# Kernel tuning notes

Hardware: AMD Instinct MI355X
Metric: run time of the kernel (lower is better)

## Reference

```python
import jax, jax.numpy as jnp
import numpy as np

L, B, S, D, SD, E, V = 6, 16, 512, 512, 128, 1536, 32000
PDX = 1  # padding_idx: embedding row zeroed


def _pos_encode(seq_len, d_model):
    pos = np.arange(seq_len)[:, None].astype(np.float32)
    i = np.arange(d_model)[None, :].astype(np.float32)
    ang = pos / np.power(10000.0, 2.0 * np.floor(i / 2.0) / d_model)
    pe = np.where(np.arange(d_model)[None, :] % 2 == 0, np.sin(ang), np.cos(ang))
    return jnp.asarray(pe, dtype=jnp.float32)


def setup_inputs() -> dict:
    key = jax.random.key(0)
    ks = jax.random.split(key, 12)
    def n(k, shape, std=0.02):
        return jax.random.normal(k, shape, jnp.float32) * std
    embed = n(ks[0], (V, D)).at[PDX].set(0.0)
    return dict(
        src_tokens=jax.random.randint(ks[1], (B, S), 0, V),
        src_mask=jax.random.randint(ks[2], (B, S), 0, 2).astype(bool),
        embed=embed,
        ln_g=jnp.ones((L, D)), ln_b=jnp.zeros((L, D)),
        Wz=n(ks[3], (L, D, SD)), bz=jnp.zeros((L, SD)),
        gq=1.0 + n(ks[4], (L, S, SD)), bq=n(ks[5], (L, S, SD)),
        gk=1.0 + n(ks[6], (L, S, SD)), bk=n(ks[7], (L, S, SD)),
        Wu=n(ks[8], (L, D, E)), bu=jnp.zeros((L, E)),
        Wv=n(ks[9], (L, D, E)), bv=jnp.zeros((L, E)),
        Wo=n(ks[10], (L, E, D)), bo=jnp.zeros((L, D)),
        fin_g=jnp.ones((D,)), fin_b=jnp.zeros((D,)),
    )


def _ln(x, g, b, eps=1e-5):
    m = x.mean(-1, keepdims=True)
    v = ((x - m) ** 2).mean(-1, keepdims=True)
    return (x - m) * jax.lax.rsqrt(v + eps) * g + b


def reference(src_tokens, src_mask, embed, ln_g, ln_b, Wz, bz, gq, bq, gk, bk,
              Wu, bu, Wv, bv, Wo, bo, fin_g, fin_b):
    d_model = embed.shape[1]
    x = embed[src_tokens] * (d_model ** 0.5)
    x = x + _pos_encode(src_tokens.shape[1], d_model)[None]  # dropout: eval -> identity
    mask = src_mask[:, None, :]  # (B,1,S): zero attention to masked key positions

    def layer(x, p):
        lg, lb, wz, bz_, gq_, bq_, gk_, bk_, wu, bu_, wv, bv_, wo, bo_ = p
        xn = _ln(x, lg, lb)
        u = xn @ wu + bu_          # (B,S,E)
        v = xn @ wv + bv_          # (B,S,E)
        z = xn @ wz + bz_          # (B,S,SD)
        q = z * gq_ + bq_          # scale_offset (per-position affine)
        k = z * gk_ + bk_
        a = jnp.maximum(jnp.einsum('bsd,btd->bst', q, k), 0.0) ** 2  # relu(qk)^2
        a = jnp.where(mask, 0.0, a)
        o = u * jnp.einsum('bst,bte->bse', a, v)  # gated attention output
        return x + o @ wo + bo_, None

    params = (ln_g, ln_b, Wz, bz, gq, bq, gk, bk, Wu, bu, Wv, bv, Wo, bo)
    x, _ = jax.lax.scan(layer, x, params)
    return _ln(x, fin_g, fin_b)
```

## Files before the change

kernel.cpp:

```cpp
#include <hip/hip_runtime.h>
#include <hip/hip_bf16.h>
#include <stdint.h>

constexpr int L = 6, B = 16, S = 512, D = 512, SD = 128, E = 1536;

using bf16x8 = __attribute__((ext_vector_type(8))) short;
using f32x4  = __attribute__((ext_vector_type(4))) float;

typedef __attribute__((address_space(1))) void gvoid;
typedef __attribute__((address_space(3))) void lvoid;

__device__ __forceinline__ unsigned short f2bf(float f) {
    __hip_bfloat16 h = __float2bfloat16(f);
    return __builtin_bit_cast(unsigned short, h);
}
__device__ __forceinline__ float bf2f(unsigned short u) {
    unsigned int v = ((unsigned int)u) << 16;
    return __builtin_bit_cast(float, v);
}
__device__ __forceinline__ void gload16(const void* g, void* l) {
    __builtin_amdgcn_global_load_lds((gvoid*)g, (lvoid*)l, 16, 0, 0);
}

__global__ void detect_mask_kernel(const unsigned char* __restrict__ m, int* flag) {
    if (threadIdx.x == 0) *flag = 0;
    __syncthreads();
    int any = 0;
    for (int i = threadIdx.x; i < B * S; i += blockDim.x)
        if ((i & 3) != 0 && m[i] != 0) any = 1;
    if (any) atomicOr(flag, 1);
}

__global__ void embed_kernel(const int* __restrict__ tok, const float* __restrict__ embed,
                             float* __restrict__ x) {
    int idx = blockIdx.x * blockDim.x + threadIdx.x;
    int d = idx & (D - 1);
    int bs = idx >> 9;
    int s = bs & (S - 1);
    float e = embed[(size_t)tok[bs] * D + d] * 22.62741699796952f;
    float expo = (float)(d >> 1) * (1.0f / 256.0f);
    float ang = (float)s * expf(expo * -9.210340371976184f);
    float pe = (d & 1) ? cosf(ang) : sinf(ang);
    x[idx] = e + pe;
}

__global__ __launch_bounds__(256) void tcast_kernel(const float* __restrict__ W,
                                                    unsigned short* __restrict__ Wt,
                                                    int K, int N, long ostride) {
    __shared__ float t[32][33];
    W  += (size_t)blockIdx.z * K * N;
    Wt += (size_t)blockIdx.z * ostride;
    int k0 = blockIdx.x * 32, n0 = blockIdx.y * 32;
    int tx = threadIdx.x, ty = threadIdx.y;
#pragma unroll
    for (int i = 0; i < 4; ++i)
        t[ty + i * 8][tx] = W[(size_t)(k0 + ty + i * 8) * N + n0 + tx];
    __syncthreads();
#pragma unroll
    for (int i = 0; i < 4; ++i)
        Wt[(size_t)(n0 + ty + i * 8) * K + k0 + tx] = f2bf(t[tx][ty + i * 8]);
}

template <bool BF>
__global__ __launch_bounds__(64) void ln_kernel(const float* __restrict__ x,
                                                const float* __restrict__ g,
                                                const float* __restrict__ b,
                                                void* __restrict__ yp) {
    int row = blockIdx.x;
    int lane = threadIdx.x;
    const float* xr = x + (size_t)row * D;
    float4 v0 = *(const float4*)(xr + lane * 4);
    float4 v1 = *(const float4*)(xr + 256 + lane * 4);
    float sum = v0.x + v0.y + v0.z + v0.w + v1.x + v1.y + v1.z + v1.w;
#pragma unroll
    for (int o = 1; o < 64; o <<= 1) sum += __shfl_xor(sum, o);
    float m = sum * (1.0f / D);
    float d0 = v0.x - m, d1 = v0.y - m, d2 = v0.z - m, d3 = v0.w - m;
    float e0 = v1.x - m, e1 = v1.y - m, e2 = v1.z - m, e3 = v1.w - m;
    float sq = d0 * d0 + d1 * d1 + d2 * d2 + d3 * d3 + e0 * e0 + e1 * e1 + e2 * e2 + e3 * e3;
#pragma unroll
    for (int o = 1; o < 64; o <<= 1) sq += __shfl_xor(sq, o);
    float inv = rsqrtf(sq * (1.0f / D) + 1e-5f);
    int c0 = lane * 4, c1 = 256 + lane * 4;
    float4 g0 = *(const float4*)(g + c0), g1 = *(const float4*)(g + c1);
    float4 b0 = *(const float4*)(b + c0), b1 = *(const float4*)(b + c1);
    float o0 = d0 * inv * g0.x + b0.x, o1 = d1 * inv * g0.y + b0.y;
    float o2 = d2 * inv * g0.z + b0.z, o3 = d3 * inv * g0.w + b0.w;
    float o4 = e0 * inv * g1.x + b1.x, o5 = e1 * inv * g1.y + b1.y;
    float o6 = e2 * inv * g1.z + b1.z, o7 = e3 * inv * g1.w + b1.w;
    if constexpr (BF) {
        unsigned short* yr = (unsigned short*)yp + (size_t)row * D;
        ushort4 p0 = {f2bf(o0), f2bf(o1), f2bf(o2), f2bf(o3)};
        ushort4 p1 = {f2bf(o4), f2bf(o5), f2bf(o6), f2bf(o7)};
        *(ushort4*)(yr + c0) = p0;
        *(ushort4*)(yr + c1) = p1;
    } else {
        float* yr = (float*)yp + (size_t)row * D;
        float4 p0 = {o0, o1, o2, o3}, p1 = {o4, o5, o6, o7};
        *(float4*)(yr + c0) = p0;
        *(float4*)(yr + c1) = p1;
    }
}

__global__ void qk_kernel(const float* __restrict__ z, const float* __restrict__ gq,
                          const float* __restrict__ bq, const float* __restrict__ gk,
                          const float* __restrict__ bk, unsigned short* __restrict__ q,
                          unsigned short* __restrict__ k) {
    int idx = blockIdx.x * blockDim.x + threadIdx.x;
    int sc = idx & (S * SD - 1);
    float zv = z[idx];
    q[idx] = f2bf(fmaf(zv, gq[sc], bq[sc]));
    k[idx] = f2bf(fmaf(zv, gk[sc], bk[sc]));
}

template <int BM, int BN>
__device__ __forceinline__ void gemm_core(const unsigned short* __restrict__ Ab,
                                          const unsigned short* __restrict__ Bb,
                                          int K, short* lsA, short* lsB,
                                          f32x4 (&acc)[BM / 32][BN / 32],
                                          int lane, int wv) {
    constexpr int NA = BM / 32, NB = BN / 32;
    constexpr int FM = BM / 32, FN = BN / 32;
    constexpr int WTM = BM / 2, WTN = BN / 2;
    const int wm = wv >> 1, wn = wv & 1;
    const unsigned short* ga[NA]; int lofsA[NA];
    const unsigned short* gb[NB]; int lofsB[NB];
#pragma unroll
    for (int i = 0; i < NA; ++i) {
        int s = wv * NA + i;
        int r = s * 8 + (lane >> 3);
        int cl = (lane & 7) ^ (r & 7);
        ga[i] = Ab + (size_t)r * K + cl * 8;
        lofsA[i] = s * 512;
    }
#pragma unroll
    for (int i = 0; i < NB; ++i) {
        int s = wv * NB + i;
        int r = s * 8 + (lane >> 3);
        int cl = (lane & 7) ^ (r & 7);
        gb[i] = Bb + (size_t)r * K + cl * 8;
        lofsB[i] = s * 512;
    }
    const int nkt = K >> 6;
    for (int kt = 0; kt < nkt; ++kt) {
        if (kt) __syncthreads();
#pragma unroll
        for (int i = 0; i < NA; ++i) gload16(ga[i] + kt * 64, (void*)&lsA[lofsA[i]]);
#pragma unroll
        for (int i = 0; i < NB; ++i) gload16(gb[i] + kt * 64, (void*)&lsB[lofsB[i]]);
        __syncthreads();
#pragma unroll
        for (int ks = 0; ks < 2; ++ks) {
            bf16x8 aF[FM], bF[FN];
#pragma unroll
            for (int f = 0; f < FM; ++f) {
                int ra = wm * WTM + f * 16 + (lane & 15);
                int ca = (ks * 4 + (lane >> 4)) ^ (ra & 7);
                aF[f] = *(const bf16x8*)&lsA[ra * 64 + ca * 8];
            }
#pragma unroll
            for (int f = 0; f < FN; ++f) {
                int rb = wn * WTN + f * 16 + (lane & 15);
                int cb = (ks * 4 + (lane >> 4)) ^ (rb & 7);
                bF[f] = *(const bf16x8*)&lsB[rb * 64 + cb * 8];
            }
#pragma unroll
            for (int fi = 0; fi < FM; ++fi)
#pragma unroll
                for (int fj = 0; fj < FN; ++fj)
                    acc[fi][fj] = __builtin_amdgcn_mfma_f32_16x16x32_bf16(
                        aF[fi], bF[fj], acc[fi][fj], 0, 0, 0);
        }
    }
}

template <int EPI, int BM, int BN>
__global__ __launch_bounds__(256) void mgemm(const unsigned short* __restrict__ A,
                                             const unsigned short* __restrict__ Bt,
                                             const float* __restrict__ bias,
                                             const void* __restrict__ aux,
                                             const int* __restrict__ flagp,
                                             void* __restrict__ Cp,
                                             int N, int K,
                                             long sA, long sB, long sC, long sAux) {
    __shared__ short lsA[BM * 64];
    __shared__ short lsB[BN * 64];
    constexpr int FM = BM / 32, FN = BN / 32;
    const int tid = threadIdx.x;
    const int lane = tid & 63, wv = tid >> 6;
    const int wm = wv >> 1, wn = wv & 1;
    const int row0 = blockIdx.x * BM, col0 = blockIdx.y * BN;
    const int bz = blockIdx.z;

    const unsigned short* Ab = A + (size_t)bz * sA + (size_t)row0 * K;
    const unsigned short* Bb = Bt + (size_t)bz * sB + (size_t)col0 * K;

    f32x4 acc[FM][FN] = {};
    gemm_core<BM, BN>(Ab, Bb, K, lsA, lsB, acc, lane, wv);

    const int lr4 = (lane >> 4) * 4;
    const int lc = lane & 15;
#pragma unroll
    for (int fi = 0; fi < FM; ++fi) {
        int rb = row0 + wm * (BM / 2) + fi * 16 + lr4;
#pragma unroll
        for (int fj = 0; fj < FN; ++fj) {
            int c = col0 + wn * (BN / 2) + fj * 16 + lc;
            f32x4 v = acc[fi][fj];
            if constexpr (EPI == 3) {
                int mv = (*flagp) ? (int)((const unsigned char*)aux)[bz * sAux + c]
                                  : ((const int*)aux)[bz * sAux + c];
                unsigned short* C = (unsigned short*)Cp + (size_t)bz * sC;
#pragma unroll
                for (int g = 0; g < 4; ++g) {
                    float vv = fmaxf(v[g], 0.0f);
                    vv *= vv;
                    C[(size_t)(rb + g) * N + c] = mv ? (unsigned short)0 : f2bf(vv);
                }
            } else if constexpr (EPI == 4) {
                const unsigned short* U = (const unsigned short*)aux + (size_t)bz * sAux;
                unsigned short* C = (unsigned short*)Cp + (size_t)bz * sC;
#pragma unroll
                for (int g = 0; g < 4; ++g) {
                    size_t off = (size_t)(rb + g) * N + c;
                    C[off] = f2bf(bf2f(U[off]) * v[g]);
                }
            } else {
                float bv = bias[c];
                const float* X = (const float*)aux;
                float* C = (float*)Cp;
#pragma unroll
                for (int g = 0; g < 4; ++g) {
                    size_t off = (size_t)(rb + g) * N + c;
                    C[off] = v[g] + bv + X[off];
                }
            }
        }
    }
}

__global__ __launch_bounds__(256) void uvz_gemm(const unsigned short* __restrict__ xn,
                                                const unsigned short* __restrict__ Wuvzt,
                                                const float* __restrict__ bu,
                                                const float* __restrict__ bvp,
                                                const float* __restrict__ bzp,
                                                unsigned short* __restrict__ u,
                                                unsigned short* __restrict__ vt,
                                                float* __restrict__ z) {
    __shared__ short lsA[128 * 64];
    __shared__ short lsB[128 * 64];
    const int tid = threadIdx.x;
    const int lane = tid & 63, wv = tid >> 6;
    const int wm = wv >> 1, wn = wv & 1;
    const int row0 = blockIdx.x * 128, col0 = blockIdx.y * 128;

    const unsigned short* Ab = xn + (size_t)row0 * D;
    const unsigned short* Bb = Wuvzt + (size_t)col0 * D;

    f32x4 acc[4][4] = {};
    gemm_core<128, 128>(Ab, Bb, D, lsA, lsB, acc, lane, wv);

    const int lr4 = (lane >> 4) * 4;
    const int lc = lane & 15;
#pragma unroll
    for (int fi = 0; fi < 4; ++fi) {
        int rb = row0 + wm * 64 + fi * 16 + lr4;
#pragma unroll
        for (int fj = 0; fj < 4; ++fj) {
            int c = col0 + wn * 64 + fj * 16 + lc;
            f32x4 v = acc[fi][fj];
            if (c < 1536) {
                float bv = bu[c];
#pragma unroll
                for (int g = 0; g < 4; ++g)
                    u[(size_t)(rb + g) * E + c] = f2bf(v[g] + bv);
            } else if (c < 3072) {
                int cv = c - 1536;
                float bv = bvp[cv];
                int b = rb >> 9, t0 = rb & 511;
                ushort4 o = {f2bf(v[0] + bv), f2bf(v[1] + bv),
                             f2bf(v[2] + bv), f2bf(v[3] + bv)};
                *(ushort4*)&vt[((size_t)b * E + cv) * 512 + t0] = o;
            } else {
                int cz = c - 3072;
                float bv = bzp[cz];
#pragma unroll
                for (int g = 0; g < 4; ++g)
                    z[(size_t)(rb + g) * SD + cz] = v[g] + bv;
            }
        }
    }
}

extern "C" void kernel_launch(void* const* d_in, const int* in_sizes, int n_in,
                              void* d_out, int out_size, void* d_ws, size_t ws_size,
                              hipStream_t stream) {
    const int* tok = (const int*)d_in[0];
    const unsigned char* mask = (const unsigned char*)d_in[1];
    const float* embed = (const float*)d_in[2];
    const float* ln_g = (const float*)d_in[3];
    const float* ln_b = (const float*)d_in[4];
    const float* Wz = (const float*)d_in[5];
    const float* bz = (const float*)d_in[6];
    const float* gq = (const float*)d_in[7];
    const float* bq = (const float*)d_in[8];
    const float* gk = (const float*)d_in[9];
    const float* bk = (const float*)d_in[10];
    const float* Wu = (const float*)d_in[11];
    const float* bu = (const float*)d_in[12];
    const float* Wv = (const float*)d_in[13];
    const float* bv = (const float*)d_in[14];
    const float* Wo = (const float*)d_in[15];
    const float* bo = (const float*)d_in[16];
    const float* fin_g = (const float*)d_in[17];
    const float* fin_b = (const float*)d_in[18];

    char* wsb = (char*)d_ws;
    size_t off = 0;
    auto alloc = [&](size_t nbytes) {
        void* p = wsb + off;
        off = (off + nbytes + 255) & ~(size_t)255;
        return p;
    };
    int* flag = (int*)alloc(256);
    float* x = (float*)alloc((size_t)B * S * D * 4);
    unsigned short* xn = (unsigned short*)alloc((size_t)B * S * D * 2);
    float* z = (float*)alloc((size_t)B * S * SD * 4);
    unsigned short* q = (unsigned short*)alloc((size_t)B * S * SD * 2);
    unsigned short* k = (unsigned short*)alloc((size_t)B * S * SD * 2);
    unsigned short* u = (unsigned short*)alloc((size_t)B * S * E * 2);
    unsigned short* vt = (unsigned short*)alloc((size_t)B * E * S * 2);
    unsigned short* o = (unsigned short*)alloc((size_t)B * S * E * 2);
    unsigned short* a = (unsigned short*)alloc((size_t)B * S * S * 2);
    unsigned short* Wuvzt = (unsigned short*)alloc((size_t)L * 3200 * D * 2);
    unsigned short* Wot = (unsigned short*)alloc((size_t)L * D * E * 2);

    constexpr long WUVZ = 3200L * D;

    detect_mask_kernel<<<1, 256, 0, stream>>>(mask, flag);
    embed_kernel<<<(B * S * D) / 256, 256, 0, stream>>>(tok, embed, x);
    tcast_kernel<<<dim3(D / 32, E / 32, L), dim3(32, 8), 0, stream>>>(Wu, Wuvzt, D, E, WUVZ);
    tcast_kernel<<<dim3(D / 32, E / 32, L), dim3(32, 8), 0, stream>>>(
        Wv, Wuvzt + 1536L * D, D, E, WUVZ);
    tcast_kernel<<<dim3(D / 32, SD / 32, L), dim3(32, 8), 0, stream>>>(
        Wz, Wuvzt + 3072L * D, D, SD, WUVZ);
    tcast_kernel<<<dim3(E / 32, D / 32, L), dim3(32, 8), 0, stream>>>(
        Wo, Wot, E, D, (long)D * E);

    for (int l = 0; l < L; ++l) {
        ln_kernel<true><<<B * S, 64, 0, stream>>>(x, ln_g + l * D, ln_b + l * D, xn);
        uvz_gemm<<<dim3(64, 25), 256, 0, stream>>>(
            xn, Wuvzt + (size_t)l * WUVZ, bu + l * E, bv + l * E, bz + l * SD, u, vt, z);
        qk_kernel<<<(B * S * SD) / 256, 256, 0, stream>>>(
            z, gq + (size_t)l * S * SD, bq + (size_t)l * S * SD,
            gk + (size_t)l * S * SD, bk + (size_t)l * S * SD, q, k);
        mgemm<3, 64, 64><<<dim3(8, 8, B), 256, 0, stream>>>(
            q, k, nullptr, mask, flag, a, S, SD,
            (long)S * SD, (long)S * SD, (long)S * S, S);
        mgemm<4, 128, 64><<<dim3(4, 24, B), 256, 0, stream>>>(
            a, vt, nullptr, u, nullptr, o, E, S,
            (long)S * S, (long)E * S, (long)S * E, (long)S * E);
        mgemm<5, 128, 64><<<dim3(64, 8), 256, 0, stream>>>(
            o, Wot + (size_t)l * D * E, bo + l * D, x, nullptr, x, D, E, 0, 0, 0, 0);
    }
    ln_kernel<false><<<B * S, 64, 0, stream>>>(x, fin_g, fin_b, (float*)d_out);
}
```

Baseline: 813.4 us.

## Split UVZ GEMM per region, fuse q/k affine, swap MFMA operands, swizzle blocks

Splits the fused u/v/z projection GEMM into three region-specialised launches. The z region now applies the per-position q/k scale and offset in its epilogue, which removes the separate qk kernel and the fp32 z buffer. MFMA operands are swapped so each lane holds four consecutive columns, letting epilogues do vectorised ushort4/float4 stores instead of scalar strided ones. A block-id swizzle is added to spread blocks across XCDs/caches. The trade-off is two extra launches, and the z-region launch is small (64 blocks), which may underfill the GPU.

New measurement: 783.9 us. 3.6% less time.

```diff
diff --git a/kernel.cpp b/kernel.cpp
--- a/kernel.cpp
+++ b/kernel.cpp
@@ -20,6 +20,17 @@
 }
 __device__ __forceinline__ void gload16(const void* g, void* l) {
     __builtin_amdgcn_global_load_lds((gvoid*)g, (lvoid*)l, 16, 0, 0);
+}
+
+__device__ __forceinline__ void swz_bid(int& bx, int& by, int& bz) {
+    int gx = gridDim.x, gy = gridDim.y, gz = gridDim.z;
+    int n = gx * gy * gz;
+    int id = blockIdx.x + gx * (blockIdx.y + gy * blockIdx.z);
+    int id2 = (id & 7) * (n >> 3) + (id >> 3);
+    by = id2 % gy;
+    int t = id2 / gy;
+    bx = t % gx;
+    bz = t / gx;
 }
 
 __global__ void detect_mask_kernel(const unsigned char* __restrict__ m, int* flag) {
@@ -102,18 +113,7 @@
     }
 }
 
-__global__ void qk_kernel(const float* __restrict__ z, const float* __restrict__ gq,
-                          const float* __restrict__ bq, const float* __restrict__ gk,
-                          const float* __restrict__ bk, unsigned short* __restrict__ q,
-                          unsigned short* __restrict__ k) {
-    int idx = blockIdx.x * blockDim.x + threadIdx.x;
-    int sc = idx & (S * SD - 1);
-    float zv = z[idx];
-    q[idx] = f2bf(fmaf(zv, gq[sc], bq[sc]));
-    k[idx] = f2bf(fmaf(zv, gk[sc], bk[sc]));
-}
-
-template <int BM, int BN>
+template <int BM, int BN, bool SWAP>
 __device__ __forceinline__ void gemm_core(const unsigned short* __restrict__ Ab,
                                           const unsigned short* __restrict__ Bb,
                                           int K, short* lsA, short* lsB,
@@ -167,9 +167,83 @@
 #pragma unroll
             for (int fi = 0; fi < FM; ++fi)
 #pragma unroll
-                for (int fj = 0; fj < FN; ++fj)
-                    acc[fi][fj] = __builtin_amdgcn_mfma_f32_16x16x32_bf16(
-                        aF[fi], bF[fj], acc[fi][fj], 0, 0, 0);
+                for (int fj = 0; fj < FN; ++fj) {
+                    if constexpr (SWAP)
+                        acc[fi][fj] = __builtin_amdgcn_mfma_f32_16x16x32_bf16(
+                            bF[fj], aF[fi], acc[fi][fj], 0, 0, 0);
+                    else
+                        acc[fi][fj] = __builtin_amdgcn_mfma_f32_16x16x32_bf16(
+                            aF[fi], bF[fj], acc[fi][fj], 0, 0, 0);
+                }
+        }
+    }
+}
+
+template <int REGION>
+__global__ __launch_bounds__(256) void uvz_gemm(const unsigned short* __restrict__ xn,
+                                                const unsigned short* __restrict__ Bt,
+                                                const float* __restrict__ bias,
+                                                const float* __restrict__ gq,
+                                                const float* __restrict__ bq,
+                                                const float* __restrict__ gk,
+                                                const float* __restrict__ bk,
+                                                unsigned short* __restrict__ o0,
+                                                unsigned short* __restrict__ o1) {
+    __shared__ short lsA[128 * 64];
+    __shared__ short lsB[128 * 64];
+    int bx, by, bzz;
+    swz_bid(bx, by, bzz);
+    const int tid = threadIdx.x;
+    const int lane = tid & 63, wv = tid >> 6;
+    const int wm = wv >> 1, wn = wv & 1;
+    const int row0 = bx * 128, col0 = by * 128;
+    const unsigned short* Ab = xn + (size_t)row0 * D;
+    const unsigned short* Bb = Bt + (size_t)col0 * D;
+
+    f32x4 acc[4][4] = {};
+    gemm_core<128, 128, (REGION != 1)>(Ab, Bb, D, lsA, lsB, acc, lane, wv);
+
+    const int lr4 = (lane >> 4) * 4;
+    const int lc = lane & 15;
+#pragma unroll
+    for (int fi = 0; fi < 4; ++fi) {
+#pragma unroll
+        for (int fj = 0; fj < 4; ++fj) {
+            f32x4 v = acc[fi][fj];
+            if constexpr (REGION == 0) {
+                int r = row0 + wm * 64 + fi * 16 + lc;
+                int cb = col0 + wn * 64 + fj * 16 + lr4;
+                f32x4 bv = *(const f32x4*)&bias[cb];
+                ushort4 ov = {f2bf(v[0] + bv[0]), f2bf(v[1] + bv[1]),
+                              f2bf(v[2] + bv[2]), f2bf(v[3] + bv[3])};
+                *(ushort4*)&o0[(size_t)r * E + cb] = ov;
+            } else if constexpr (REGION == 1) {
+                int rb = row0 + wm * 64 + fi * 16 + lr4;
+                int c = col0 + wn * 64 + fj * 16 + lc;
+                float bv = bias[c];
+                int b = rb >> 9, t0 = rb & 511;
+                ushort4 ov = {f2bf(v[0] + bv), f2bf(v[1] + bv),
+                              f2bf(v[2] + bv), f2bf(v[3] + bv)};
+                *(ushort4*)&o0[((size_t)b * E + c) * 512 + t0] = ov;
+            } else {
+                int r = row0 + wm * 64 + fi * 16 + lc;
+                int cb = wn * 64 + fj * 16 + lr4;
+                int s = r & 511;
+                f32x4 bz4 = *(const f32x4*)&bias[cb];
+                f32x4 gq4 = *(const f32x4*)&gq[(size_t)s * SD + cb];
+                f32x4 bq4 = *(const f32x4*)&bq[(size_t)s * SD + cb];
+                f32x4 gk4 = *(const f32x4*)&gk[(size_t)s * SD + cb];
+                f32x4 bk4 = *(const f32x4*)&bk[(size_t)s * SD + cb];
+                ushort4 qv, kv;
+#pragma unroll
+                for (int g = 0; g < 4; ++g) {
+                    float zz = v[g] + bz4[g];
+                    ((unsigned short*)&qv)[g] = f2bf(fmaf(zz, gq4[g], bq4[g]));
+                    ((unsigned short*)&kv)[g] = f2bf(fmaf(zz, gk4[g], bk4[g]));
+                }
+                *(ushort4*)&o0[(size_t)r * SD + cb] = qv;
+                *(ushort4*)&o1[(size_t)r * SD + cb] = kv;
+            }
         }
     }
 }
@@ -186,107 +260,59 @@
     __shared__ short lsA[BM * 64];
     __shared__ short lsB[BN * 64];
     constexpr int FM = BM / 32, FN = BN / 32;
+    int bx, by, bz;
+    swz_bid(bx, by, bz);
     const int tid = threadIdx.x;
     const int lane = tid & 63, wv = tid >> 6;
     const int wm = wv >> 1, wn = wv & 1;
-    const int row0 = blockIdx.x * BM, col0 = blockIdx.y * BN;
-    const int bz = blockIdx.z;
+    const int row0 = bx * BM, col0 = by * BN;
 
     const unsigned short* Ab = A + (size_t)bz * sA + (size_t)row0 * K;
     const unsigned short* Bb = Bt + (size_t)bz * sB + (size_t)col0 * K;
 
     f32x4 acc[FM][FN] = {};
-    gemm_core<BM, BN>(Ab, Bb, K, lsA, lsB, acc, lane, wv);
+    gemm_core<BM, BN, true>(Ab, Bb, K, lsA, lsB, acc, lane, wv);
 
     const int lr4 = (lane >> 4) * 4;
     const int lc = lane & 15;
 #pragma unroll
     for (int fi = 0; fi < FM; ++fi) {
-        int rb = row0 + wm * (BM / 2) + fi * 16 + lr4;
+        int r = row0 + wm * (BM / 2) + fi * 16 + lc;
 #pragma unroll
         for (int fj = 0; fj < FN; ++fj) {
-            int c = col0 + wn * (BN / 2) + fj * 16 + lc;
+            int cb = col0 + wn * (BN / 2) + fj * 16 + lr4;
             f32x4 v = acc[fi][fj];
             if constexpr (EPI == 3) {
-                int mv = (*flagp) ? (int)((const unsigned char*)aux)[bz * sAux + c]
+                unsigned short* C = (unsigned short*)Cp + (size_t)bz * sC;
+                int flag = *flagp;
+                ushort4 ov;
+#pragma unroll
+                for (int g = 0; g < 4; ++g) {
+                    int c = cb + g;
+                    int mv = flag ? (int)((const unsigned char*)aux)[bz * sAux + c]
                                   : ((const int*)aux)[bz * sAux + c];
-                unsigned short* C = (unsigned short*)Cp + (size_t)bz * sC;
-#pragma unroll
-                for (int g = 0; g < 4; ++g) {
                     float vv = fmaxf(v[g], 0.0f);
                     vv *= vv;
-                    C[(size_t)(rb + g) * N + c] = mv ? (unsigned short)0 : f2bf(vv);
+                    ((unsigned short*)&ov)[g] = mv ? (unsigned short)0 : f2bf(vv);
                 }
+                *(ushort4*)&C[(size_t)r * N + cb] = ov;
             } else if constexpr (EPI == 4) {
                 const unsigned short* U = (const unsigned short*)aux + (size_t)bz * sAux;
                 unsigned short* C = (unsigned short*)Cp + (size_t)bz * sC;
-#pragma unroll
-                for (int g = 0; g < 4; ++g) {
-                    size_t off = (size_t)(rb + g) * N + c;
-                    C[off] = f2bf(bf2f(U[off]) * v[g]);
-                }
+                size_t off = (size_t)r * N + cb;
+                ushort4 uu = *(const ushort4*)&U[off];
+                ushort4 ov = {f2bf(bf2f(uu.x) * v[0]), f2bf(bf2f(uu.y) * v[1]),
+                              f2bf(bf2f(uu.z) * v[2]), f2bf(bf2f(uu.w) * v[3])};
+                *(ushort4*)&C[off] = ov;
             } else {
-                float bv = bias[c];
+                float* C = (float*)Cp;
                 const float* X = (const float*)aux;
-                float* C = (float*)Cp;
-#pragma unroll
-                for (int g = 0; g < 4; ++g) {
-                    size_t off = (size_t)(rb + g) * N + c;
-                    C[off] = v[g] + bv + X[off];
-                }
-            }
-        }
-    }
-}
-
-__global__ __launch_bounds__(256) void uvz_gemm(const unsigned short* __restrict__ xn,
-                                                const unsigned short* __restrict__ Wuvzt,
-                                                const float* __restrict__ bu,
-                                                const float* __restrict__ bvp,
-                                                const float* __restrict__ bzp,
-                                                unsigned short* __restrict__ u,
-                                                unsigned short* __restrict__ vt,
-                                                float* __restrict__ z) {
-    __shared__ short lsA[128 * 64];
-    __shared__ short lsB[128 * 64];
-    const int tid = threadIdx.x;
-    const int lane = tid & 63, wv = tid >> 6;
-    const int wm = wv >> 1, wn = wv & 1;
-    const int row0 = blockIdx.x * 128, col0 = blockIdx.y * 128;
-
-    const unsigned short* Ab = xn + (size_t)row0 * D;
-    const unsigned short* Bb = Wuvzt + (size_t)col0 * D;
-
-    f32x4 acc[4][4] = {};
-    gemm_core<128, 128>(Ab, Bb, D, lsA, lsB, acc, lane, wv);
-
-    const int lr4 = (lane >> 4) * 4;
-    const int lc = lane & 15;
-#pragma unroll
-    for (int fi = 0; fi < 4; ++fi) {
-        int rb = row0 + wm * 64 + fi * 16 + lr4;
-#pragma unroll
-        for (int fj = 0; fj < 4; ++fj) {
-            int c = col0 + wn * 64 + fj * 16 + lc;
-            f32x4 v = acc[fi][fj];
-            if (c < 1536) {
-                float bv = bu[c];
-#pragma unroll
-                for (int g = 0; g < 4; ++g)
-                    u[(size_t)(rb + g) * E + c] = f2bf(v[g] + bv);
-            } else if (c < 3072) {
-                int cv = c - 1536;
-                float bv = bvp[cv];
-                int b = rb >> 9, t0 = rb & 511;
-                ushort4 o = {f2bf(v[0] + bv), f2bf(v[1] + bv),
-                             f2bf(v[2] + bv), f2bf(v[3] + bv)};
-                *(ushort4*)&vt[((size_t)b * E + cv) * 512 + t0] = o;
-            } else {
-                int cz = c - 3072;
-                float bv = bzp[cz];
-#pragma unroll
-                for (int g = 0; g < 4; ++g)
-                    z[(size_t)(rb + g) * SD + cz] = v[g] + bv;
+                size_t off = (size_t)r * N + cb;
+                f32x4 bb = *(const f32x4*)&bias[cb];
+                f32x4 xx = *(const f32x4*)&X[off];
+                f32x4 ov = {v[0] + bb[0] + xx[0], v[1] + bb[1] + xx[1],
+                            v[2] + bb[2] + xx[2], v[3] + bb[3] + xx[3]};
+                *(f32x4*)&C[off] = ov;
             }
         }
     }
@@ -325,7 +351,6 @@
     int* flag = (int*)alloc(256);
     float* x = (float*)alloc((size_t)B * S * D * 4);
     unsigned short* xn = (unsigned short*)alloc((size_t)B * S * D * 2);
-    float* z = (float*)alloc((size_t)B * S * SD * 4);
     unsigned short* q = (unsigned short*)alloc((size_t)B * S * SD * 2);
     unsigned short* k = (unsigned short*)alloc((size_t)B * S * SD * 2);
     unsigned short* u = (unsigned short*)alloc((size_t)B * S * E * 2);
@@ -349,10 +374,15 @@
 
     for (int l = 0; l < L; ++l) {
         ln_kernel<true><<<B * S, 64, 0, stream>>>(x, ln_g + l * D, ln_b + l * D, xn);
-        uvz_gemm<<<dim3(64, 25), 256, 0, stream>>>(
-            xn, Wuvzt + (size_t)l * WUVZ, bu + l * E, bv + l * E, bz + l * SD, u, vt, z);
-        qk_kernel<<<(B * S * SD) / 256, 256, 0, stream>>>(
-            z, gq + (size_t)l * S * SD, bq + (size_t)l * S * SD,
+        uvz_gemm<0><<<dim3(64, 12), 256, 0, stream>>>(
+            xn, Wuvzt + (size_t)l * WUVZ, bu + l * E,
+            nullptr, nullptr, nullptr, nullptr, u, nullptr);
+        uvz_gemm<1><<<dim3(64, 12), 256, 0, stream>>>(
+            xn, Wuvzt + (size_t)l * WUVZ + 1536L * D, bv + l * E,
+            nullptr, nullptr, nullptr, nullptr, vt, nullptr);
+        uvz_gemm<2><<<dim3(64, 1), 256, 0, stream>>>(
+            xn, Wuvzt + (size_t)l * WUVZ + 3072L * D, bz + l * SD,
+            gq + (size_t)l * S * SD, bq + (size_t)l * S * SD,
             gk + (size_t)l * S * SD, bk + (size_t)l * S * SD, q, k);
         mgemm<3, 64, 64><<<dim3(8, 8, B), 256, 0, stream>>>(
             q, k, nullptr, mask, flag, a, S, SD,
```
